# Kernel tuning notes

Hardware: AMD Instinct MI355X
Metric: run time of the kernel (lower is better)

The kernel has to match this reference:

```python
import jax, jax.numpy as jnp
import numpy as np

INPUT_SHAPE = 640
NUM_CLASSES = 80
STRIDES = (8, 16, 32)
DIS = 2.5 * STRIDES[0]        # center-region half-size (pixels)
EPS = 1e-7
BIG = 1e5                      # penalty for non-(center&inbox) candidates
INF = 1e9                      # effectively excludes a pair from top-k / argmin
BS, MAX_GT, NGT_VALID = 32, 50, 20


def _bce(p, t):
    p = jnp.clip(p, EPS, 1.0 - EPS)
    return -t * jnp.log(p) - (1.0 - t) * jnp.log(1.0 - p)


def _decode(pred, stride):
    # pred [B, 5+nc, l, l] -> decoded [B, l*l, 5+nc] with boxes in pixels (cx,cy,w,h)
    B, C, l, _ = pred.shape
    p = jnp.transpose(pred, (0, 2, 3, 1))          # [B, l, l, C] (row=y, col=x)
    xy = jax.nn.sigmoid(p[..., :2])
    wh = p[..., 2:4]
    objcls = jax.nn.sigmoid(p[..., 4:])
    gx = jnp.arange(l, dtype=p.dtype)[None, :]      # ix varies along width
    gy = jnp.arange(l, dtype=p.dtype)[:, None]      # iy varies along height
    x = (gx + xy[..., 0]) * stride
    y = (gy + xy[..., 1]) * stride
    w = jnp.exp(wh[..., 0]) * stride
    h = jnp.exp(wh[..., 1]) * stride
    out = jnp.concatenate([jnp.stack([x, y, w, h], -1), objcls], -1)
    return out.reshape(B, l * l, C)


def _pairwise_iou(gt, pr):
    # gt [G,4], pr [A,4] in cxcywh -> [G,A]
    g_tl = gt[:, None, :2] - gt[:, None, 2:4] * 0.5
    g_br = gt[:, None, :2] + gt[:, None, 2:4] * 0.5
    p_tl = pr[None, :, :2] - pr[None, :, 2:4] * 0.5
    p_br = pr[None, :, :2] + pr[None, :, 2:4] * 0.5
    wh = jnp.maximum(jnp.minimum(g_br, p_br) - jnp.maximum(g_tl, p_tl), 0.0)
    inter = wh[..., 0] * wh[..., 1]
    union = gt[:, None, 2] * gt[:, None, 3] + pr[None, :, 2] * pr[None, :, 3] - inter
    return inter / jnp.clip(union, 1e-6)


def _region_mask(px, py, cx, cy, hw, hh):
    # anchor center inside (clipped) box around (cx,cy) with half-extents (hw,hh)
    left = jnp.maximum(cx - hw, 0.0)[:, None]
    right = jnp.minimum(cx + hw, float(INPUT_SHAPE))[:, None]
    top = jnp.maximum(cy - hh, 0.0)[:, None]
    bot = jnp.minimum(cy + hh, float(INPUT_SHAPE))[:, None]
    return (px[None] >= left) & (px[None] <= right) & (py[None] >= top) & (py[None] <= bot)


def _per_image(pred, tgt):
    # pred [A, 5+nc] decoded, tgt [G, 5+nc]
    G, A = tgt.shape[0], pred.shape[0]
    valid = tgt[:, 4] == 1.0
    px, py = pred[:, 0], pred[:, 1]
    cx, cy, gw, gh = tgt[:, 0], tgt[:, 1], tgt[:, 2], tgt[:, 3]

    center_m = _region_mask(px, py, cx, cy, DIS, DIS)
    inbox_m = _region_mask(px, py, cx, cy, gw * 0.5, gh * 0.5)
    or_m = (center_m | inbox_m) & valid[:, None]     # candidate anchors
    and_m = center_m & inbox_m & valid[:, None]      # preferred anchors

    iou = _pairwise_iou(tgt[:, :4], pred[:, :4])     # [G, A]
    iou_cost = -jnp.log(iou + 1e-8)

    # pairwise class BCE cost summed over classes, via matmul (one-hot targets)
    pcls = jnp.clip(pred[:, 5:], EPS, 1.0 - EPS)     # [A, nc]
    logp = jnp.log(pcls)
    log1mp = jnp.log(1.0 - pcls)
    tcls = tgt[:, 5:]                                 # [G, nc]
    cls_cost = tcls @ (log1mp - logp).T - log1mp.sum(-1)[None, :]  # [G, A]

    cost = cls_cost + 3.0 * iou_cost + BIG * (~and_m)
    cost_full = jnp.where(valid[:, None], cost, INF)
    cost_sel = jnp.where(or_m, cost, INF)

    # dynamic-k: sum of top-10 candidate IoUs, floored at 1, capped by #and-candidates
    k10 = jax.lax.top_k(iou * or_m.astype(iou.dtype), 10)[0].sum(-1)
    and_cnt = and_m.sum(-1)
    dk = jnp.minimum(jnp.maximum(k10.astype(jnp.int32), 1), jnp.maximum(and_cnt, 1))

    # take 10 lowest-cost anchors per GT, keep the first dk of them
    _, topi = jax.lax.top_k(-cost_sel, 10)            # [G, 10]
    keep = (jnp.arange(10)[None, :] < dk[:, None]) & valid[:, None]
    keep = keep & jnp.take_along_axis(or_m, topi, axis=1)
    assign = jnp.zeros((G, A), jnp.int32).at[jnp.arange(G)[:, None], topi].max(
        keep.astype(jnp.int32)) > 0                    # [G, A] bool

    overlap = assign.sum(0) > 1
    best = jnp.argmin(cost_full, axis=0)              # [A]
    onehot = jnp.arange(G)[:, None] == best[None, :]
    assign = jnp.where(overlap[None, :], onehot, assign)

    fg = assign.any(0)
    l_conf = _bce(pred[:, 4], fg.astype(pred.dtype)).sum()
    l_cls = jnp.sum(jnp.where(assign, cls_cost, 0.0))
    l_reg = jnp.sum(jnp.where(assign, 1.0 - iou ** 2, 0.0))
    return l_reg, l_conf, l_cls, valid.sum()


def setup_inputs() -> dict:
    key = jax.random.key(0)
    k1, k2, k3, k4, k5, k6, k7 = jax.random.split(key, 7)
    p8 = 0.5 * jax.random.normal(k1, (BS, 5 + NUM_CLASSES, 80, 80), jnp.float32)
    p16 = 0.5 * jax.random.normal(k2, (BS, 5 + NUM_CLASSES, 40, 40), jnp.float32)
    p32 = 0.5 * jax.random.normal(k3, (BS, 5 + NUM_CLASSES, 20, 20), jnp.float32)
    # targets: (cx, cy, w, h, valid_flag, one_hot_class)
    cxy = jax.random.uniform(k4, (BS, NGT_VALID, 2), jnp.float32, 32.0, INPUT_SHAPE - 32.0)
    wh = jax.random.uniform(k5, (BS, NGT_VALID, 2), jnp.float32, 16.0, 128.0)
    cls_idx = jax.random.randint(k6, (BS, NGT_VALID), 0, NUM_CLASSES)
    onehot = jax.nn.one_hot(cls_idx, NUM_CLASSES, dtype=jnp.float32)
    flag = jnp.ones((BS, NGT_VALID, 1), jnp.float32)
    valid_rows = jnp.concatenate([cxy, wh, flag, onehot], -1)   # [BS, 20, 85]
    pad = jnp.zeros((BS, MAX_GT - NGT_VALID, 5 + NUM_CLASSES), jnp.float32)
    targets = jnp.concatenate([valid_rows, pad], axis=1)        # [BS, 50, 85]
    return {"p8": p8, "p16": p16, "p32": p32, "targets": targets}


def reference(p8, p16, p32, targets):
    preds = jnp.concatenate(
        [_decode(p8, STRIDES[0]), _decode(p16, STRIDES[1]), _decode(p32, STRIDES[2])],
        axis=1)                                                  # [BS, 8400, 85]
    l_reg, l_conf, l_cls, ng = jax.vmap(_per_image)(preds, targets)
    num_gts = jnp.maximum(ng.sum(), 1).astype(preds.dtype)
    reg_weight = 5.0
    return (reg_weight * l_reg.sum() + l_cls.sum() + l_conf.sum()) / num_gts
```

## Files before the change

kernel.cpp:

```cpp
#include <hip/hip_runtime.h>
#include <math.h>

#define BSZ  32
#define GSZ  50
#define ATOT 8400
#define NCLS 80
#define CDIM 85
#define TPB  256
#define GRIDX ((ATOT + TPB - 1) / TPB)
#define NPART (GRIDX * BSZ)
#define MAXC 512

#define EPSF 1e-7f
#define BIGF 100000.0f
#define INFF 1000000000.0f
#define IMGF 640.0f
#define DISF 20.0f
#define LOGEPS_HI -15.942385f

__device__ __forceinline__ float fexp(float x){ return __expf(x); }
__device__ __forceinline__ float flog(float x){ return __logf(x); }

__device__ __forceinline__ float sigm(float z){ return 1.0f/(1.0f+fexp(-z)); }
__device__ __forceinline__ float clampp(float s){ return fminf(fmaxf(s, EPSF), 1.f-EPSF); }
__device__ __forceinline__ float log1msig(float z){
  return fmaxf(-flog(1.f + fexp(z)), LOGEPS_HI);
}

__device__ __forceinline__ const float* chan_ptr(const float* __restrict__ p8,
                                                 const float* __restrict__ p16,
                                                 const float* __restrict__ p32,
                                                 int b, int a, int ch){
  if (a < 6400) return p8  + ((size_t)(b*CDIM + ch))*6400 + a;
  if (a < 8000) return p16 + ((size_t)(b*CDIM + ch))*1600 + (a-6400);
  return p32 + ((size_t)(b*CDIM + ch))*400 + (a-8000);
}

__device__ __forceinline__ void compute_pair(
  float cx, float cy, float gw, float gh,
  float px, float py, float pw, float ph,
  float z, float slog,
  float& cost, float& iou, bool& orm, bool& andm, float& clsc)
{
  float hw = gw*0.5f, hh = gh*0.5f;
  bool cm = (px >= fmaxf(cx-DISF,0.f)) && (px <= fminf(cx+DISF,IMGF)) &&
            (py >= fmaxf(cy-DISF,0.f)) && (py <= fminf(cy+DISF,IMGF));
  bool im = (px >= fmaxf(cx-hw,0.f)) && (px <= fminf(cx+hw,IMGF)) &&
            (py >= fmaxf(cy-hh,0.f)) && (py <= fminf(cy+hh,IMGF));
  orm = cm || im;  andm = cm && im;
  float phw = pw*0.5f, phh = ph*0.5f;
  float wx = fmaxf(fminf(cx+hw, px+phw) - fmaxf(cx-hw, px-phw), 0.f);
  float wy = fmaxf(fminf(cy+hh, py+phh) - fmaxf(cy-hh, py-phh), 0.f);
  float inter = wx*wy;
  float uni   = gw*gh + pw*ph - inter;
  iou = inter / fmaxf(uni, 1e-6f);
  clsc = -z - slog;
  cost = clsc + 3.f*(-flog(iou + 1e-8f)) + (andm ? 0.f : BIGF);
}

__global__ void k_prep(const float* __restrict__ tgt, int* __restrict__ cidx){
  int t = blockIdx.x*blockDim.x + threadIdx.x;
  if (t >= BSZ*GSZ) return;
  const float* T = tgt + (size_t)t*CDIM;
  int best = 0; float bv = T[5];
  for (int c = 1; c < NCLS; c++){
    float v = T[5+c];
    if (v > bv){ bv = v; best = c; }
  }
  cidx[t] = best;
}

__global__ void k_decode(const float* __restrict__ p8, const float* __restrict__ p16,
                         const float* __restrict__ p32,
                         float* __restrict__ bx, float* __restrict__ by,
                         float* __restrict__ bw, float* __restrict__ bh,
                         float* __restrict__ obj, float* __restrict__ slog,
                         unsigned long long* __restrict__ bits){
  int t = blockIdx.x*blockDim.x + threadIdx.x;
  int sub = t & 3;
  int g   = t >> 2;
  int b = g / (ATOT/4);
  int q = g % (ATOT/4);
  int a0 = q*4;
  const float* base; int l; float fs; int aL;
  if (a0 < 6400){ base = p8;  l = 80; fs = 8.f;  aL = a0; }
  else if (a0 < 8000){ base = p16; l = 40; fs = 16.f; aL = a0-6400; }
  else { base = p32; l = 20; fs = 32.f; aL = a0-8000; }
  int l2 = l*l;
  int cs = l2 >> 2;
  const float4* p4 = (const float4*)(base + (size_t)b*CDIM*l2) + (aL >> 2);

  float4 S = make_float4(0.f,0.f,0.f,0.f);
  for (int c = 5+sub; c < CDIM; c += 4){
    float4 v = p4[c*cs];
    S.x += log1msig(v.x); S.y += log1msig(v.y);
    S.z += log1msig(v.z); S.w += log1msig(v.w);
  }
  #pragma unroll
  for (int m = 1; m <= 2; m <<= 1){
    S.x += __shfl_xor(S.x, m, 64);
    S.y += __shfl_xor(S.y, m, 64);
    S.z += __shfl_xor(S.z, m, 64);
    S.w += __shfl_xor(S.w, m, 64);
  }

  int i = aL / l, j = aL % l;
  float fi = (float)i;
  uint4 z4 = make_uint4(0u,0u,0u,0u);
  if (sub == 0){
    float4 v0 = p4[0];
    float4 v4 = p4[4*cs];
    ((float4*)bx)[g]  = make_float4(((float)(j  )+sigm(v0.x))*fs, ((float)(j+1)+sigm(v0.y))*fs,
                                    ((float)(j+2)+sigm(v0.z))*fs, ((float)(j+3)+sigm(v0.w))*fs);
    ((float4*)obj)[g] = make_float4(sigm(v4.x), sigm(v4.y), sigm(v4.z), sigm(v4.w));
    ((uint4*)bits)[2*g] = z4;
  } else if (sub == 1){
    float4 v1 = p4[cs];
    ((float4*)by)[g]   = make_float4((fi+sigm(v1.x))*fs, (fi+sigm(v1.y))*fs,
                                     (fi+sigm(v1.z))*fs, (fi+sigm(v1.w))*fs);
    ((float4*)slog)[g] = S;
  } else if (sub == 2){
    float4 v2 = p4[2*cs];
    ((float4*)bw)[g] = make_float4(fexp(v2.x)*fs, fexp(v2.y)*fs, fexp(v2.z)*fs, fexp(v2.w)*fs);
    ((uint4*)bits)[2*g+1] = z4;
  } else {
    float4 v3 = p4[3*cs];
    ((float4*)bh)[g] = make_float4(fexp(v3.x)*fs, fexp(v3.y)*fs, fexp(v3.z)*fs, fexp(v3.w)*fs);
  }
}

__global__ void k_assign(const float* __restrict__ p8, const float* __restrict__ p16,
                         const float* __restrict__ p32, const float* __restrict__ tgt,
                         const int* __restrict__ cidx,
                         const float* __restrict__ bx, const float* __restrict__ by,
                         const float* __restrict__ bw, const float* __restrict__ bh,
                         const float* __restrict__ slog,
                         unsigned long long* __restrict__ bits){
  int g = blockIdx.x, b = blockIdx.y;
  const float* T = tgt + ((size_t)b*GSZ + g)*CDIM;
  if (T[4] != 1.0f) return;
  float cx = T[0], cy = T[1], gw = T[2], gh = T[3];
  float hw = gw*0.5f, hh = gh*0.5f;
  float cL = fmaxf(cx-DISF,0.f), cR = fminf(cx+DISF,IMGF);
  float cT = fmaxf(cy-DISF,0.f), cB = fminf(cy+DISF,IMGF);
  float iL = fmaxf(cx-hw,0.f),  iR = fminf(cx+hw,IMGF);
  float iT = fmaxf(cy-hh,0.f),  iB = fminf(cy+hh,IMGF);
  float gArea = gw*gh;
  int ch = 5 + cidx[b*GSZ + g];
  int t = threadIdx.x;
  int lane = t & 63, wave = t >> 6;

  const float* BX = bx + (size_t)b*ATOT;
  const float* BY = by + (size_t)b*ATOT;
  const float* BW = bw + (size_t)b*ATOT;
  const float* BH = bh + (size_t)b*ATOT;
  const float* SL = slog + (size_t)b*ATOT;

  __shared__ int cand[MAXC];
  __shared__ int ncand_sh, nand_sh;
  if (t == 0){ ncand_sh = 0; nand_sh = 0; }
  __syncthreads();
  for (int a = t; a < ATOT; a += TPB){
    float px = BX[a], py = BY[a];
    bool cm = (px >= cL) && (px <= cR) && (py >= cT) && (py <= cB);
    bool im = (px >= iL) && (px <= iR) && (py >= iT) && (py <= iB);
    if (cm || im){
      int pos = atomicAdd(&ncand_sh, 1);
      if (pos < MAXC) cand[pos] = a | ((cm && im) ? 0x10000 : 0);
      if (cm && im) atomicAdd(&nand_sh, 1);
    }
  }
  __syncthreads();
  int nc = ncand_sh < MAXC ? ncand_sh : MAXC;
  int and_cnt = nand_sh;

  float lc[10]; int li[10]; float lio[10];
  #pragma unroll
  for (int k = 0; k < 10; k++){ lc[k] = 3.0e38f; li[k] = -1; lio[k] = -1.f; }

  for (int c = t; c < nc; c += TPB){
    int packed = cand[c];
    int a = packed & 0xFFFF;
    bool andm = (packed & 0x10000) != 0;
    float px = BX[a], py = BY[a];
    float pw = BW[a], ph = BH[a];
    float phw = pw*0.5f, phh = ph*0.5f;
    float wx = fmaxf(fminf(cx+hw, px+phw) - fmaxf(cx-hw, px-phw), 0.f);
    float wy = fmaxf(fminf(cy+hh, py+phh) - fmaxf(cy-hh, py-phh), 0.f);
    float inter = wx*wy;
    float iou = inter / fmaxf(gArea + pw*ph - inter, 1e-6f);
    float z = *chan_ptr(p8, p16, p32, b, a, ch);
    float clsc = -z - SL[a];
    float cost = clsc + 3.f*(-flog(iou + 1e-8f)) + (andm ? 0.f : BIGF);
    {
      float v = cost; int vi = a;
      #pragma unroll
      for (int k = 0; k < 10; k++){
        if (v < lc[k] || (v == lc[k] && (unsigned)vi < (unsigned)li[k])){
          float tv = lc[k]; int ti = li[k];
          lc[k] = v; li[k] = vi; v = tv; vi = ti;
        }
      }
    }
    if (iou > lio[9]){
      float v = iou;
      #pragma unroll
      for (int k = 0; k < 10; k++){
        if (v > lio[k]){ float tv = lio[k]; lio[k] = v; v = tv; }
      }
    }
  }

  float mc[10]; int mi[10]; float mio[10];
  {
    int hp = 0;
    #pragma unroll
    for (int r = 0; r < 10; r++){
      float v  = (hp < 10) ? lc[hp] : 3.4e38f;
      int  idx = (hp < 10) ? li[hp] : -1;
      int  wl  = lane;
      #pragma unroll
      for (int s2 = 32; s2 > 0; s2 >>= 1){
        float v2 = __shfl_xor(v, s2, 64);
        int   i2 = __shfl_xor(idx, s2, 64);
        int   l2 = __shfl_xor(wl, s2, 64);
        if (v2 < v || (v2 == v && (unsigned)i2 < (unsigned)idx)){
          v = v2; idx = i2; wl = l2;
        }
      }
      mc[r] = v; mi[r] = idx;
      if (lane == wl) hp++;
    }
    int hq = 0;
    #pragma unroll
    for (int r = 0; r < 10; r++){
      float v = (hq < 10) ? lio[hq] : -2.f;
      int  wl = lane;
      #pragma unroll
      for (int s2 = 32; s2 > 0; s2 >>= 1){
        float v2 = __shfl_xor(v, s2, 64);
        int   l2 = __shfl_xor(wl, s2, 64);
        if (v2 > v || (v2 == v && l2 < wl)){ v = v2; wl = l2; }
      }
      mio[r] = v;
      if (lane == wl) hq++;
    }
  }

  __shared__ float smc[4*10]; __shared__ int smi[4*10]; __shared__ float smio[4*10];
  if (lane == 0){
    #pragma unroll
    for (int k = 0; k < 10; k++){
      smc[wave*10+k] = mc[k]; smi[wave*10+k] = mi[k]; smio[wave*10+k] = mio[k];
    }
  }
  __syncthreads();

  if (t == 0){
    float k10 = 0.f;
    {
      int h[4] = {0,0,0,0};
      for (int r = 0; r < 10; r++){
        float v = -2.f; int w = -1;
        for (int q = 0; q < 4; q++){
          if (h[q] < 10){
            float vq = smio[q*10+h[q]];
            if (vq > v){ v = vq; w = q; }
          }
        }
        if (w >= 0) h[w]++;
        k10 += fmaxf(v, 0.f);
      }
    }
    int dk = (int)k10;
    if (dk < 1) dk = 1;
    int ub = and_cnt > 1 ? and_cnt : 1;
    if (dk > ub) dk = ub;
    int h[4] = {0,0,0,0};
    for (int r = 0; r < dk && r < 10; r++){
      float v = 3.4e38f; int idx = -1; int w = -1;
      for (int q = 0; q < 4; q++){
        if (h[q] < 10){
          float vq = smc[q*10+h[q]]; int iq = smi[q*10+h[q]];
          if (vq < v || (vq == v && (unsigned)iq < (unsigned)idx)){
            v = vq; idx = iq; w = q;
          }
        }
      }
      if (idx < 0) break;
      h[w]++;
      atomicOr(&bits[(size_t)b*ATOT + idx], 1ull << g);
    }
  }
}

__global__ void k_loss(const float* __restrict__ p8, const float* __restrict__ p16,
                       const float* __restrict__ p32, const float* __restrict__ tgt,
                       const int* __restrict__ cidx,
                       const float* __restrict__ bx, const float* __restrict__ by,
                       const float* __restrict__ bw, const float* __restrict__ bh,
                       const float* __restrict__ obj, const float* __restrict__ slog,
                       const unsigned long long* __restrict__ bits,
                       float* __restrict__ partials){
  int b = blockIdx.y;
  int a = blockIdx.x*TPB + threadIdx.x;
  __shared__ float gcx[GSZ], gcy[GSZ], ggw[GSZ], ggh[GSZ], gval[GSZ];
  __shared__ int gci[GSZ];
  for (int k = threadIdx.x; k < GSZ; k += TPB){
    const float* T = tgt + ((size_t)b*GSZ + k)*CDIM;
    gcx[k] = T[0]; gcy[k] = T[1]; ggw[k] = T[2]; ggh[k] = T[3]; gval[k] = T[4];
    gci[k] = cidx[b*GSZ + k];
  }
  __syncthreads();

  float contrib = 0.f;
  if (a < ATOT){
    size_t t = (size_t)b*ATOT + a;
    unsigned long long m = bits[t];
    float o = clampp(obj[t]);
    if (m == 0ull){
      contrib = -flog(1.f - o);
    } else {
      float px = bx[t], py = by[t], pw = bw[t], ph = bh[t], sl = slog[t];
      if (__builtin_popcountll(m) > 1){
        float bestc = INFF; int bestg = 0;
        for (int g = 0; g < GSZ; g++){
          float c = INFF;
          if (gval[g] == 1.0f){
            float z = *chan_ptr(p8, p16, p32, b, a, 5+gci[g]);
            float iou, clsc; bool orm, andm;
            compute_pair(gcx[g], gcy[g], ggw[g], ggh[g], px, py, pw, ph, z, sl,
                         c, iou, orm, andm, clsc);
          }
          if (c < bestc){ bestc = c; bestg = g; }
        }
        m = 1ull << bestg;
      }
      contrib = -flog(o);
      while (m){
        int g = __builtin_ctzll(m);
        m &= m - 1;
        float z = *chan_ptr(p8, p16, p32, b, a, 5+gci[g]);
        float c, iou, clsc; bool orm, andm;
        compute_pair(gcx[g], gcy[g], ggw[g], ggh[g], px, py, pw, ph, z, sl,
                     c, iou, orm, andm, clsc);
        contrib += clsc + 5.f*(1.f - iou*iou);
      }
    }
  }

  #pragma unroll
  for (int s2 = 32; s2 > 0; s2 >>= 1) contrib += __shfl_xor(contrib, s2, 64);
  __shared__ float wsum[4];
  if ((threadIdx.x & 63) == 0) wsum[threadIdx.x >> 6] = contrib;
  __syncthreads();
  if (threadIdx.x == 0)
    partials[blockIdx.y*GRIDX + blockIdx.x] = wsum[0]+wsum[1]+wsum[2]+wsum[3];
}

__global__ void k_final(const float* __restrict__ partials,
                        const float* __restrict__ tgt, float* __restrict__ out){
  int t = threadIdx.x;
  float s = 0.f;
  for (int i = t; i < NPART; i += TPB) s += partials[i];
  int n = 0;
  for (int i = t; i < BSZ*GSZ; i += TPB)
    n += (tgt[(size_t)i*CDIM + 4] == 1.0f) ? 1 : 0;
  __shared__ float sh[TPB]; __shared__ int shn[TPB];
  sh[t] = s; shn[t] = n;
  __syncthreads();
  for (int st = TPB/2; st > 0; st >>= 1){
    if (t < st){ sh[t] += sh[t+st]; shn[t] += shn[t+st]; }
    __syncthreads();
  }
  if (t == 0){
    int nn = shn[0] < 1 ? 1 : shn[0];
    out[0] = sh[0] / (float)nn;
  }
}

extern "C" void kernel_launch(void* const* d_in, const int* in_sizes, int n_in,
                              void* d_out, int out_size, void* d_ws, size_t ws_size,
                              hipStream_t stream) {
  const float* p8  = (const float*)d_in[0];
  const float* p16 = (const float*)d_in[1];
  const float* p32 = (const float*)d_in[2];
  const float* tgt = (const float*)d_in[3];
  float* out = (float*)d_out;

  const size_t BA = (size_t)BSZ*ATOT;
  float* bx   = (float*)d_ws;
  float* by   = bx + BA;
  float* bw   = by + BA;
  float* bh   = bw + BA;
  float* obj  = bh + BA;
  float* slog = obj + BA;
  unsigned long long* bits = (unsigned long long*)(slog + BA);
  int* cidx = (int*)(bits + BA);
  float* partials = (float*)(cidx + BSZ*GSZ);

  dim3 blk(TPB);
  k_prep  <<<dim3((BSZ*GSZ + TPB-1)/TPB), blk, 0, stream>>>(tgt, cidx);
  k_decode<<<dim3((unsigned)(BA/TPB)), blk, 0, stream>>>(p8, p16, p32,
                                                   bx, by, bw, bh, obj, slog, bits);
  k_assign<<<dim3(GSZ, BSZ), blk, 0, stream>>>(p8, p16, p32, tgt, cidx,
                                               bx, by, bw, bh, slog, bits);
  k_loss  <<<dim3(GRIDX, BSZ), blk, 0, stream>>>(p8, p16, p32, tgt, cidx,
                                               bx, by, bw, bh, obj, slog, bits, partials);
  k_final <<<1, blk, 0, stream>>>(partials, tgt, out);
}
```

Baseline: 184.4 us.

## Restrict assignment scan to bounding grid rectangles and use bitonic wave top-k

The assign kernel now scans only the grid cells inside each GT's bounding rectangle at every FPN level, instead of all 8400 anchors. Candidate compaction uses ballot-based, warp-aggregated atomics. The per-thread insertion top-k is replaced by packing cost and index into a 64-bit key and running a wave-level bitonic sort, with the block raised to 512 threads. The k_prep kernel is folded into k_decode to save a launch. The cost is that only the first 512 candidates are processed, each with one thread, and the rectangle bounds must be exact to avoid missing anchors.

```diff
diff --git a/kernel.cpp b/kernel.cpp
--- a/kernel.cpp
+++ b/kernel.cpp
@@ -7,6 +7,7 @@
 #define NCLS 80
 #define CDIM 85
 #define TPB  256
+#define TPA  512
 #define GRIDX ((ATOT + TPB - 1) / TPB)
 #define NPART (GRIDX * BSZ)
 #define MAXC 512
@@ -58,24 +59,12 @@
   cost = clsc + 3.f*(-flog(iou + 1e-8f)) + (andm ? 0.f : BIGF);
 }
 
-__global__ void k_prep(const float* __restrict__ tgt, int* __restrict__ cidx){
-  int t = blockIdx.x*blockDim.x + threadIdx.x;
-  if (t >= BSZ*GSZ) return;
-  const float* T = tgt + (size_t)t*CDIM;
-  int best = 0; float bv = T[5];
-  for (int c = 1; c < NCLS; c++){
-    float v = T[5+c];
-    if (v > bv){ bv = v; best = c; }
-  }
-  cidx[t] = best;
-}
-
 __global__ void k_decode(const float* __restrict__ p8, const float* __restrict__ p16,
-                         const float* __restrict__ p32,
+                         const float* __restrict__ p32, const float* __restrict__ tgt,
                          float* __restrict__ bx, float* __restrict__ by,
                          float* __restrict__ bw, float* __restrict__ bh,
                          float* __restrict__ obj, float* __restrict__ slog,
-                         unsigned long long* __restrict__ bits){
+                         unsigned long long* __restrict__ bits, int* __restrict__ cidx){
   int t = blockIdx.x*blockDim.x + threadIdx.x;
   int sub = t & 3;
   int g   = t >> 2;
@@ -127,15 +116,31 @@
     float4 v3 = p4[3*cs];
     ((float4*)bh)[g] = make_float4(fexp(v3.x)*fs, fexp(v3.y)*fs, fexp(v3.z)*fs, fexp(v3.w)*fs);
   }
-}
-
-__global__ void k_assign(const float* __restrict__ p8, const float* __restrict__ p16,
-                         const float* __restrict__ p32, const float* __restrict__ tgt,
-                         const int* __restrict__ cidx,
-                         const float* __restrict__ bx, const float* __restrict__ by,
-                         const float* __restrict__ bw, const float* __restrict__ bh,
-                         const float* __restrict__ slog,
-                         unsigned long long* __restrict__ bits){
+
+  if (t < BSZ*GSZ){
+    const float* Tq = tgt + (size_t)t*CDIM;
+    int best = 0; float bv = Tq[5];
+    for (int c = 1; c < NCLS; c++){
+      float vv = Tq[5+c];
+      if (vv > bv){ bv = vv; best = c; }
+    }
+    cidx[t] = best;
+  }
+}
+
+__device__ __forceinline__ unsigned f2u(float f){
+  unsigned u = __float_as_uint(f);
+  return (u & 0x80000000u) ? ~u : (u | 0x80000000u);
+}
+
+__global__ __launch_bounds__(TPA)
+void k_assign(const float* __restrict__ p8, const float* __restrict__ p16,
+              const float* __restrict__ p32, const float* __restrict__ tgt,
+              const int* __restrict__ cidx,
+              const float* __restrict__ bx, const float* __restrict__ by,
+              const float* __restrict__ bw, const float* __restrict__ bh,
+              const float* __restrict__ slog,
+              unsigned long long* __restrict__ bits){
   int g = blockIdx.x, b = blockIdx.y;
   const float* T = tgt + ((size_t)b*GSZ + g)*CDIM;
   if (T[4] != 1.0f) return;
@@ -156,30 +161,61 @@
   const float* BH = bh + (size_t)b*ATOT;
   const float* SL = slog + (size_t)b*ATOT;
 
+  float ux = fmaxf(DISF, hw), uy = fmaxf(DISF, hh);
+  float RL = fmaxf(cx-ux, 0.f), RR = fminf(cx+ux, IMGF);
+  float RT = fmaxf(cy-uy, 0.f), RB = fminf(cy+uy, IMGF);
+
+  auto rect = [&](float inv, int l, int& j0r, int& i0r, int& wr, int& hr){
+    int a_ = (int)floorf(RL*inv) - 1; if (a_ < 0) a_ = 0;
+    int b_ = (int)floorf(RR*inv) + 1; if (b_ > l-1) b_ = l-1;
+    int c_ = (int)floorf(RT*inv) - 1; if (c_ < 0) c_ = 0;
+    int d_ = (int)floorf(RB*inv) + 1; if (d_ > l-1) d_ = l-1;
+    j0r = a_; i0r = c_; wr = b_-a_+1; hr = d_-c_+1;
+  };
+  int j0_0,i0_0,w_0,h_0, j0_1,i0_1,w_1,h_1, j0_2,i0_2,w_2,h_2;
+  rect(0.125f,   80, j0_0,i0_0,w_0,h_0);
+  rect(0.0625f,  40, j0_1,i0_1,w_1,h_1);
+  rect(0.03125f, 20, j0_2,i0_2,w_2,h_2);
+  int o1 = w_0*h_0, o2 = o1 + w_1*h_1, ntot = o2 + w_2*h_2;
+
   __shared__ int cand[MAXC];
-  __shared__ int ncand_sh, nand_sh;
-  if (t == 0){ ncand_sh = 0; nand_sh = 0; }
-  __syncthreads();
-  for (int a = t; a < ATOT; a += TPB){
+  __shared__ int ncand_sh;
+  __shared__ int wand[TPA/64];
+  if (t == 0) ncand_sh = 0;
+  __syncthreads();
+
+  int myand = 0;
+  for (int cell = t; cell < ntot; cell += TPA){
+    int v = (cell >= o1) + (cell >= o2);
+    int loc, jj0, ii0, ww, ll, ab;
+    if (v == 0){ loc = cell;    jj0=j0_0; ii0=i0_0; ww=w_0; ll=80; ab=0;    }
+    else if (v == 1){ loc = cell-o1; jj0=j0_1; ii0=i0_1; ww=w_1; ll=40; ab=6400; }
+    else { loc = cell-o2; jj0=j0_2; ii0=i0_2; ww=w_2; ll=20; ab=8000; }
+    int ii = ii0 + loc / ww;
+    int jj = jj0 + loc % ww;
+    int a  = ab + ii*ll + jj;
     float px = BX[a], py = BY[a];
     bool cm = (px >= cL) && (px <= cR) && (py >= cT) && (py <= cB);
     bool im = (px >= iL) && (px <= iR) && (py >= iT) && (py <= iB);
-    if (cm || im){
-      int pos = atomicAdd(&ncand_sh, 1);
-      if (pos < MAXC) cand[pos] = a | ((cm && im) ? 0x10000 : 0);
-      if (cm && im) atomicAdd(&nand_sh, 1);
-    }
-  }
+    bool orm = cm || im, andm = cm && im;
+    unsigned long long mo = __ballot(orm);
+    myand += __popcll(__ballot(andm));
+    if (orm){
+      int leader = __ffsll((long long)mo) - 1;
+      int base = 0;
+      if (lane == leader) base = atomicAdd(&ncand_sh, __popcll(mo));
+      base = __shfl(base, leader, 64);
+      int pos = base + __popcll(mo & ((1ull << lane) - 1ull));
+      if (pos < MAXC) cand[pos] = a | (andm ? 0x10000 : 0);
+    }
+  }
+  if (lane == 0) wand[wave] = myand;
   __syncthreads();
   int nc = ncand_sh < MAXC ? ncand_sh : MAXC;
-  int and_cnt = nand_sh;
-
-  float lc[10]; int li[10]; float lio[10];
-  #pragma unroll
-  for (int k = 0; k < 10; k++){ lc[k] = 3.0e38f; li[k] = -1; lio[k] = -1.f; }
-
-  for (int c = t; c < nc; c += TPB){
-    int packed = cand[c];
+
+  unsigned long long ck; float io;
+  if (t < nc){
+    int packed = cand[t];
     int a = packed & 0xFFFF;
     bool andm = (packed & 0x10000) != 0;
     float px = BX[a], py = BY[a];
@@ -188,83 +224,49 @@
     float wx = fmaxf(fminf(cx+hw, px+phw) - fmaxf(cx-hw, px-phw), 0.f);
     float wy = fmaxf(fminf(cy+hh, py+phh) - fmaxf(cy-hh, py-phh), 0.f);
     float inter = wx*wy;
-    float iou = inter / fmaxf(gArea + pw*ph - inter, 1e-6f);
+    io = inter / fmaxf(gArea + pw*ph - inter, 1e-6f);
     float z = *chan_ptr(p8, p16, p32, b, a, ch);
-    float clsc = -z - SL[a];
-    float cost = clsc + 3.f*(-flog(iou + 1e-8f)) + (andm ? 0.f : BIGF);
-    {
-      float v = cost; int vi = a;
+    float cost = (-z - SL[a]) + 3.f*(-flog(io + 1e-8f)) + (andm ? 0.f : BIGF);
+    ck = ((unsigned long long)f2u(cost) << 32) | (unsigned)a;
+  } else {
+    ck = ~0ull; io = -1.f;
+  }
+
+  __shared__ unsigned long long skey[(TPA/64)*10];
+  __shared__ float siou[(TPA/64)*10];
+  bool wactive = (wave << 6) < nc;
+  if (wactive){
+    #pragma unroll
+    for (int k = 2; k <= 64; k <<= 1){
       #pragma unroll
-      for (int k = 0; k < 10; k++){
-        if (v < lc[k] || (v == lc[k] && (unsigned)vi < (unsigned)li[k])){
-          float tv = lc[k]; int ti = li[k];
-          lc[k] = v; li[k] = vi; v = tv; vi = ti;
-        }
+      for (int j = k >> 1; j > 0; j >>= 1){
+        unsigned long long ok = __shfl_xor(ck, j, 64);
+        float oi = __shfl_xor(io, j, 64);
+        bool tmin = (((lane & k) == 0) == ((lane & j) == 0));
+        ck = tmin ? (ck < ok ? ck : ok) : (ck > ok ? ck : ok);
+        io = tmin ? fmaxf(io, oi) : fminf(io, oi);
       }
     }
-    if (iou > lio[9]){
-      float v = iou;
-      #pragma unroll
-      for (int k = 0; k < 10; k++){
-        if (v > lio[k]){ float tv = lio[k]; lio[k] = v; v = tv; }
-      }
-    }
-  }
-
-  float mc[10]; int mi[10]; float mio[10];
-  {
-    int hp = 0;
+  }
+  if (lane < 10){
+    skey[wave*10 + lane] = wactive ? ck : ~0ull;
+    siou[wave*10 + lane] = wactive ? io : -1.f;
+  }
+  __syncthreads();
+
+  if (t == 0){
+    int and_cnt = 0;
     #pragma unroll
-    for (int r = 0; r < 10; r++){
-      float v  = (hp < 10) ? lc[hp] : 3.4e38f;
-      int  idx = (hp < 10) ? li[hp] : -1;
-      int  wl  = lane;
-      #pragma unroll
-      for (int s2 = 32; s2 > 0; s2 >>= 1){
-        float v2 = __shfl_xor(v, s2, 64);
-        int   i2 = __shfl_xor(idx, s2, 64);
-        int   l2 = __shfl_xor(wl, s2, 64);
-        if (v2 < v || (v2 == v && (unsigned)i2 < (unsigned)idx)){
-          v = v2; idx = i2; wl = l2;
-        }
-      }
-      mc[r] = v; mi[r] = idx;
-      if (lane == wl) hp++;
-    }
-    int hq = 0;
-    #pragma unroll
-    for (int r = 0; r < 10; r++){
-      float v = (hq < 10) ? lio[hq] : -2.f;
-      int  wl = lane;
-      #pragma unroll
-      for (int s2 = 32; s2 > 0; s2 >>= 1){
-        float v2 = __shfl_xor(v, s2, 64);
-        int   l2 = __shfl_xor(wl, s2, 64);
-        if (v2 > v || (v2 == v && l2 < wl)){ v = v2; wl = l2; }
-      }
-      mio[r] = v;
-      if (lane == wl) hq++;
-    }
-  }
-
-  __shared__ float smc[4*10]; __shared__ int smi[4*10]; __shared__ float smio[4*10];
-  if (lane == 0){
-    #pragma unroll
-    for (int k = 0; k < 10; k++){
-      smc[wave*10+k] = mc[k]; smi[wave*10+k] = mi[k]; smio[wave*10+k] = mio[k];
-    }
-  }
-  __syncthreads();
-
-  if (t == 0){
+    for (int q = 0; q < TPA/64; q++) and_cnt += wand[q];
     float k10 = 0.f;
     {
-      int h[4] = {0,0,0,0};
+      int h[TPA/64] = {0,0,0,0,0,0,0,0};
       for (int r = 0; r < 10; r++){
         float v = -2.f; int w = -1;
-        for (int q = 0; q < 4; q++){
+        #pragma unroll
+        for (int q = 0; q < TPA/64; q++){
           if (h[q] < 10){
-            float vq = smio[q*10+h[q]];
+            float vq = siou[q*10 + h[q]];
             if (vq > v){ v = vq; w = q; }
           }
         }
@@ -276,19 +278,19 @@
     if (dk < 1) dk = 1;
     int ub = and_cnt > 1 ? and_cnt : 1;
     if (dk > ub) dk = ub;
-    int h[4] = {0,0,0,0};
+    int h[TPA/64] = {0,0,0,0,0,0,0,0};
     for (int r = 0; r < dk && r < 10; r++){
-      float v = 3.4e38f; int idx = -1; int w = -1;
-      for (int q = 0; q < 4; q++){
+      unsigned long long bestk = ~0ull; int w = -1;
+      #pragma unroll
+      for (int q = 0; q < TPA/64; q++){
         if (h[q] < 10){
-          float vq = smc[q*10+h[q]]; int iq = smi[q*10+h[q]];
-          if (vq < v || (vq == v && (unsigned)iq < (unsigned)idx)){
-            v = vq; idx = iq; w = q;
-          }
+          unsigned long long kq = skey[q*10 + h[q]];
+          if (kq < bestk){ bestk = kq; w = q; }
         }
       }
-      if (idx < 0) break;
+      if (bestk == ~0ull) break;
       h[w]++;
+      int idx = (int)(bestk & 0xFFFFFFFFull);
       atomicOr(&bits[(size_t)b*ATOT + idx], 1ull << g);
     }
   }
@@ -400,10 +402,9 @@
   float* partials = (float*)(cidx + BSZ*GSZ);
 
   dim3 blk(TPB);
-  k_prep  <<<dim3((BSZ*GSZ + TPB-1)/TPB), blk, 0, stream>>>(tgt, cidx);
-  k_decode<<<dim3((unsigned)(BA/TPB)), blk, 0, stream>>>(p8, p16, p32,
-                                                   bx, by, bw, bh, obj, slog, bits);
-  k_assign<<<dim3(GSZ, BSZ), blk, 0, stream>>>(p8, p16, p32, tgt, cidx,
+  k_decode<<<dim3((unsigned)(BA/TPB)), blk, 0, stream>>>(p8, p16, p32, tgt,
+                                                   bx, by, bw, bh, obj, slog, bits, cidx);
+  k_assign<<<dim3(GSZ, BSZ), dim3(TPA), 0, stream>>>(p8, p16, p32, tgt, cidx,
                                                bx, by, bw, bh, slog, bits);
   k_loss  <<<dim3(GRIDX, BSZ), blk, 0, stream>>>(p8, p16, p32, tgt, cidx,
                                                bx, by, bw, bh, obj, slog, bits, partials);
```

New measurement: 160.7 us. 12.9% less time.
